# Kernel optimization log

Measured on AMD Instinct MI355X. Metric: run time of the kernel, lower is better.

Reference implementation:

```python
import jax, jax.numpy as jnp
import numpy as np
import math

B, I, H = 8192, 1024, 1024

def _uniform(key, shape, lo, hi):
    return jax.random.uniform(key, shape, dtype=jnp.float32, minval=lo, maxval=hi)

def setup_inputs() -> dict:
    key = jax.random.key(0)
    ks = jax.random.split(key, 14)
    bound = math.sqrt(1.0 / H)
    lo, hi = -bound, bound
    x = jax.random.normal(ks[0], (B, I), dtype=jnp.float32)
    hid = jax.random.normal(ks[1], (B, H), dtype=jnp.float32)
    # stacked params for gates [r, z, n]
    wx = jnp.stack([_uniform(ks[2 + i], (I, H), lo, hi) for i in range(3)])   # [3, I, H]
    wh = jnp.stack([_uniform(ks[5 + i], (H, H), lo, hi) for i in range(3)])   # [3, H, H]
    bx = jnp.stack([_uniform(ks[8 + i], (H,), lo, hi) for i in range(3)])     # [3, H]
    bh = jnp.stack([_uniform(ks[11 + i], (H,), lo, hi) for i in range(3)])    # [3, H]
    return {"x": x, "hid": hid, "wx": wx, "wh": wh, "bx": bx, "bh": bh}

def reference(x, hid, wx, wh, bx, bh):
    # Fused gate projections: one big matmul per source instead of 3 small ones.
    gx = jnp.einsum('bi,gih->bgh', x, wx) + bx[None]        # [B, 3, H]
    gh = jnp.einsum('bh,ghk->bgk', hid, wh) + bh[None]      # [B, 3, H]
    r = jax.nn.sigmoid(gx[:, 0] + gh[:, 0])
    z = jax.nn.sigmoid(gx[:, 1] + gh[:, 1])
    n = jnp.tanh(gx[:, 2] + r * gh[:, 2])
    next_hid = (1.0 - z) * n + z * hid
    return next_hid
```

## Files before the change

kernel.cpp:

```cpp
#include <hip/hip_runtime.h>
#include <hip/hip_bf16.h>

typedef __hip_bfloat16 bf16;
typedef unsigned short u16;
typedef __attribute__((ext_vector_type(8))) short bf16x8;
typedef __attribute__((ext_vector_type(4))) float f32x4;
typedef __attribute__((ext_vector_type(8))) unsigned short u16x8;

#define KD 1024
#define HD 1024
#define BSZ 8192
#define BM 128
#define BN 64
#define BK 32

__device__ __forceinline__ u16 f2b(float f) {
    return __builtin_bit_cast(u16, __float2bfloat16(f));
}

__device__ __forceinline__ void gload16(const void* g, void* smem, int lds_byte_off) {
    __builtin_amdgcn_global_load_lds(
        (const __attribute__((address_space(1))) void*)g,
        (__attribute__((address_space(3))) void*)((char*)smem + lds_byte_off),
        16, 0, 0);
}

__device__ __forceinline__ bf16x8 packfrag(float4 a, float4 b) {
    bf16x8 r;
    r[0] = (short)f2b(a.x); r[1] = (short)f2b(a.y);
    r[2] = (short)f2b(a.z); r[3] = (short)f2b(a.w);
    r[4] = (short)f2b(b.x); r[5] = (short)f2b(b.y);
    r[6] = (short)f2b(b.z); r[7] = (short)f2b(b.w);
    return r;
}

__global__ __launch_bounds__(256) void transpose_w(
    const float* __restrict__ wx, const float* __restrict__ wh, u16* __restrict__ wt)
{
    __shared__ u16 tile[64][65];
    const int g = blockIdx.z;
    const float* src = (g < 3) ? (wx + (size_t)g * KD * HD) : (wh + (size_t)(g - 3) * KD * HD);
    u16* dst = wt + (size_t)g * KD * HD;
    const int r0 = blockIdx.y * 64;
    const int c0 = blockIdx.x * 64;
    const int t = threadIdx.x;

    #pragma unroll
    for (int r = 0; r < 2; r++) {
        int idx = r * 256 + t;
        int row = idx >> 3, cc = idx & 7;
        const float* p = src + (size_t)(r0 + row) * HD + c0 + cc * 8;
        #pragma unroll
        for (int e = 0; e < 8; e++) tile[row][cc * 8 + e] = f2b(p[e]);
    }
    __syncthreads();
    #pragma unroll
    for (int r = 0; r < 2; r++) {
        int idx = r * 256 + t;
        int nrow = idx >> 3, kc = idx & 7;
        u16x8 v;
        #pragma unroll
        for (int e = 0; e < 8; e++) v[e] = tile[kc * 8 + e][nrow];
        *(u16x8*)(dst + (size_t)(c0 + nrow) * KD + r0 + kc * 8) = v;
    }
}

__global__ __launch_bounds__(256, 2) void gru_fused(
    const float* __restrict__ xf, const float* __restrict__ hf,
    const u16* __restrict__ wt,
    const float* __restrict__ bxf, const float* __restrict__ bhf,
    float* __restrict__ outf)
{
    __shared__ __align__(16) char smem[57344];
    float* fx = (float*)smem;
    float* fh = (float*)(smem + 16384);
    u16*   wl = (u16*)(smem + 32768);

    const int t    = threadIdx.x;
    const int lane = t & 63;
    const int w    = t >> 6;
    const int wm   = w >> 1, wn = w & 1;
    const int quad = lane >> 4;
    const int c16  = lane & 15;
    const int lin  = blockIdx.x;
    const int nblk = (lin & 7) * 2 + ((lin >> 3) & 1);
    const int mblk = lin >> 4;
    const int m0   = mblk * BM;
    const int n0   = nblk * BN;

    const int tq = t >> 3, tc = t & 7;
    const int csrc = tc ^ (tq & 7);
    const float* gx = xf + (size_t)(m0 + tq) * KD + csrc * 4;
    const float* gh = hf + (size_t)(m0 + tq) * KD + csrc * 4;
    const u16*   gw = wt + (size_t)(n0 + (t >> 2)) * KD + (t & 3) * 8;
    const int ldsl = w * 1024;

    f32x4 acc[4][4][2];
    #pragma unroll
    for (int a = 0; a < 4; a++)
        #pragma unroll
        for (int i = 0; i < 4; i++)
            #pragma unroll
            for (int j = 0; j < 2; j++)
                acc[a][i][j] = (f32x4){0.f, 0.f, 0.f, 0.f};

    int iA0[4], iA1[4];
    #pragma unroll
    for (int i = 0; i < 4; i++) {
        int ml = wm * 64 + i * 16 + c16;
        int s  = ml & 7;
        iA0[i] = ml * 32 + ((2 * quad)     ^ s) * 4;
        iA1[i] = ml * 32 + ((2 * quad + 1) ^ s) * 4;
    }
    int iW[2];
    #pragma unroll
    for (int j = 0; j < 2; j++) {
        int nl = wn * 32 + j * 16 + c16;
        iW[j] = nl * 32 + quad * 8;
    }

    for (int k0 = 0; k0 < KD; k0 += BK) {
        #pragma unroll
        for (int r = 0; r < 4; r++)
            gload16(gx + (size_t)(32 * r) * KD, smem, r * 4096 + ldsl);
        #pragma unroll
        for (int r = 0; r < 4; r++)
            gload16(gh + (size_t)(32 * r) * KD, smem, 16384 + r * 4096 + ldsl);
        #pragma unroll
        for (int g = 0; g < 6; g++)
            gload16(gw + (size_t)g * KD * HD, smem, 32768 + g * 4096 + ldsl);
        __syncthreads();
        gx += BK; gh += BK; gw += BK;

        bf16x8 ax[4], ah[4];
        #pragma unroll
        for (int i = 0; i < 4; i++) {
            float4 u0 = *(const float4*)&fx[iA0[i]];
            float4 u1 = *(const float4*)&fx[iA1[i]];
            float4 v0 = *(const float4*)&fh[iA0[i]];
            float4 v1 = *(const float4*)&fh[iA1[i]];
            ax[i] = packfrag(u0, u1);
            ah[i] = packfrag(v0, v1);
        }
        #pragma unroll
        for (int p = 0; p < 3; p++) {
            bf16x8 bwx[2], bwh[2];
            #pragma unroll
            for (int j = 0; j < 2; j++) {
                bwx[j] = *(const bf16x8*)&wl[p * 2048       + iW[j]];
                bwh[j] = *(const bf16x8*)&wl[(p + 3) * 2048 + iW[j]];
            }
            #pragma unroll
            for (int i = 0; i < 4; i++)
                #pragma unroll
                for (int j = 0; j < 2; j++) {
                    if (p < 2) {
                        acc[p][i][j] = __builtin_amdgcn_mfma_f32_16x16x32_bf16(ax[i], bwx[j], acc[p][i][j], 0, 0, 0);
                        acc[p][i][j] = __builtin_amdgcn_mfma_f32_16x16x32_bf16(ah[i], bwh[j], acc[p][i][j], 0, 0, 0);
                    } else {
                        acc[2][i][j] = __builtin_amdgcn_mfma_f32_16x16x32_bf16(ax[i], bwx[j], acc[2][i][j], 0, 0, 0);
                        acc[3][i][j] = __builtin_amdgcn_mfma_f32_16x16x32_bf16(ah[i], bwh[j], acc[3][i][j], 0, 0, 0);
                    }
                }
        }
        __syncthreads();
    }

    float bR[2], bZ[2], bXN[2], bHN[2];
    #pragma unroll
    for (int j = 0; j < 2; j++) {
        int col = n0 + wn * 32 + j * 16 + c16;
        bR[j]  = bxf[col]          + bhf[col];
        bZ[j]  = bxf[HD + col]     + bhf[HD + col];
        bXN[j] = bxf[2 * HD + col];
        bHN[j] = bhf[2 * HD + col];
    }
    #pragma unroll
    for (int i = 0; i < 4; i++)
        #pragma unroll
        for (int j = 0; j < 2; j++) {
            int col = n0 + wn * 32 + j * 16 + c16;
            #pragma unroll
            for (int r = 0; r < 4; r++) {
                int row = m0 + wm * 64 + i * 16 + quad * 4 + r;
                size_t idx = (size_t)row * HD + col;
                float vr = acc[0][i][j][r] + bR[j];
                vr = 1.f / (1.f + __expf(-vr));
                float vz = acc[1][i][j][r] + bZ[j];
                vz = 1.f / (1.f + __expf(-vz));
                float vn = (acc[2][i][j][r] + bXN[j]) + vr * (acc[3][i][j][r] + bHN[j]);
                float e2 = __expf(2.f * vn);
                vn = 1.f - 2.f / (e2 + 1.f);
                outf[idx] = (1.f - vz) * vn + vz * hf[idx];
            }
        }
}

extern "C" void kernel_launch(void* const* d_in, const int* in_sizes, int n_in,
                              void* d_out, int out_size, void* d_ws, size_t ws_size,
                              hipStream_t stream) {
    const float* x   = (const float*)d_in[0];
    const float* hid = (const float*)d_in[1];
    const float* wx  = (const float*)d_in[2];
    const float* wh  = (const float*)d_in[3];
    const float* bx  = (const float*)d_in[4];
    const float* bh  = (const float*)d_in[5];
    float* out = (float*)d_out;

    u16* wt = (u16*)d_ws;

    dim3 tgrid(HD / 64, KD / 64, 6);
    transpose_w<<<tgrid, 256, 0, stream>>>(wx, wh, wt);
    gru_fused<<<1024, 256, 0, stream>>>(x, hid, wt, bx, bh, out);
}
```

Measured before the change: 266.0 us.

## Pre-convert activations to bf16 and load A fragments directly from global

A merged prep kernel now converts x and hid to bf16 in workspace alongside the weight transpose. The GEMM kernel reads A fragments straight from global memory into registers instead of staging fp32 tiles in LDS, and LDS shrinks to the weight tiles only. The aim is to halve A-operand traffic in the main loop, remove per-iteration fp32-to-bf16 packing, and raise occupancy. The cost is an extra full pass writing and reading the bf16 activations, plus uncoalesced 16-byte per-lane global loads with no LDS reuse across the wn warps.

```diff
diff --git a/kernel.cpp b/kernel.cpp
--- a/kernel.cpp
+++ b/kernel.cpp
@@ -14,6 +14,9 @@
 #define BN 64
 #define BK 32
 
+#define WS_XB 12582912
+#define WS_HB 29360128
+
 __device__ __forceinline__ u16 f2b(float f) {
     return __builtin_bit_cast(u16, __float2bfloat16(f));
 }
@@ -25,57 +28,62 @@
         16, 0, 0);
 }
 
-__device__ __forceinline__ bf16x8 packfrag(float4 a, float4 b) {
-    bf16x8 r;
-    r[0] = (short)f2b(a.x); r[1] = (short)f2b(a.y);
-    r[2] = (short)f2b(a.z); r[3] = (short)f2b(a.w);
-    r[4] = (short)f2b(b.x); r[5] = (short)f2b(b.y);
-    r[6] = (short)f2b(b.z); r[7] = (short)f2b(b.w);
-    return r;
-}
-
-__global__ __launch_bounds__(256) void transpose_w(
-    const float* __restrict__ wx, const float* __restrict__ wh, u16* __restrict__ wt)
+__global__ __launch_bounds__(256) void prep_all(
+    const float* __restrict__ x, const float* __restrict__ h,
+    const float* __restrict__ wx, const float* __restrict__ wh,
+    u16* __restrict__ xb, u16* __restrict__ hb, u16* __restrict__ wt)
 {
     __shared__ u16 tile[64][65];
-    const int g = blockIdx.z;
-    const float* src = (g < 3) ? (wx + (size_t)g * KD * HD) : (wh + (size_t)(g - 3) * KD * HD);
-    u16* dst = wt + (size_t)g * KD * HD;
-    const int r0 = blockIdx.y * 64;
-    const int c0 = blockIdx.x * 64;
+    const int b = blockIdx.x;
     const int t = threadIdx.x;
-
-    #pragma unroll
-    for (int r = 0; r < 2; r++) {
-        int idx = r * 256 + t;
-        int row = idx >> 3, cc = idx & 7;
-        const float* p = src + (size_t)(r0 + row) * HD + c0 + cc * 8;
-        #pragma unroll
-        for (int e = 0; e < 8; e++) tile[row][cc * 8 + e] = f2b(p[e]);
+    if (b < 3072) {
+        const int g  = b >> 9;
+        const int r0 = ((b >> 4) & 15) * 64;
+        const int c0 = (b & 15) * 64;
+        const float* src = (g < 3) ? (wx + (size_t)g * KD * HD)
+                                   : (wh + (size_t)(g - 3) * KD * HD);
+        u16* dst = wt + (size_t)g * KD * HD;
+        #pragma unroll
+        for (int r = 0; r < 2; r++) {
+            int idx = r * 256 + t;
+            int row = idx >> 3, cc = idx & 7;
+            const float* p = src + (size_t)(r0 + row) * HD + c0 + cc * 8;
+            #pragma unroll
+            for (int e = 0; e < 8; e++) tile[row][cc * 8 + e] = f2b(p[e]);
+        }
+        __syncthreads();
+        #pragma unroll
+        for (int r = 0; r < 2; r++) {
+            int idx = r * 256 + t;
+            int nrow = idx >> 3, kc = idx & 7;
+            u16x8 v;
+            #pragma unroll
+            for (int e = 0; e < 8; e++) v[e] = tile[kc * 8 + e][nrow];
+            *(u16x8*)(dst + (size_t)(c0 + nrow) * KD + r0 + kc * 8) = v;
+        }
+    } else {
+        size_t off = ((size_t)(b - 3072) * 256 + t) * 8;
+        float4 a0 = *(const float4*)(x + off);
+        float4 a1 = *(const float4*)(x + off + 4);
+        float4 b0 = *(const float4*)(h + off);
+        float4 b1 = *(const float4*)(h + off + 4);
+        u16x8 vx, vh;
+        vx[0]=f2b(a0.x); vx[1]=f2b(a0.y); vx[2]=f2b(a0.z); vx[3]=f2b(a0.w);
+        vx[4]=f2b(a1.x); vx[5]=f2b(a1.y); vx[6]=f2b(a1.z); vx[7]=f2b(a1.w);
+        vh[0]=f2b(b0.x); vh[1]=f2b(b0.y); vh[2]=f2b(b0.z); vh[3]=f2b(b0.w);
+        vh[4]=f2b(b1.x); vh[5]=f2b(b1.y); vh[6]=f2b(b1.z); vh[7]=f2b(b1.w);
+        *(u16x8*)(xb + off) = vx;
+        *(u16x8*)(hb + off) = vh;
     }
-    __syncthreads();
-    #pragma unroll
-    for (int r = 0; r < 2; r++) {
-        int idx = r * 256 + t;
-        int nrow = idx >> 3, kc = idx & 7;
-        u16x8 v;
-        #pragma unroll
-        for (int e = 0; e < 8; e++) v[e] = tile[kc * 8 + e][nrow];
-        *(u16x8*)(dst + (size_t)(c0 + nrow) * KD + r0 + kc * 8) = v;
-    }
 }
 
 __global__ __launch_bounds__(256, 2) void gru_fused(
-    const float* __restrict__ xf, const float* __restrict__ hf,
+    const u16* __restrict__ xb, const u16* __restrict__ hb,
     const u16* __restrict__ wt,
     const float* __restrict__ bxf, const float* __restrict__ bhf,
-    float* __restrict__ outf)
+    const float* __restrict__ hidf, float* __restrict__ outf)
 {
-    __shared__ __align__(16) char smem[57344];
-    float* fx = (float*)smem;
-    float* fh = (float*)(smem + 16384);
-    u16*   wl = (u16*)(smem + 32768);
-
+    __shared__ u16 wl[12288];
     const int t    = threadIdx.x;
     const int lane = t & 63;
     const int w    = t >> 6;
@@ -88,12 +96,11 @@
     const int m0   = mblk * BM;
     const int n0   = nblk * BN;
 
-    const int tq = t >> 3, tc = t & 7;
-    const int csrc = tc ^ (tq & 7);
-    const float* gx = xf + (size_t)(m0 + tq) * KD + csrc * 4;
-    const float* gh = hf + (size_t)(m0 + tq) * KD + csrc * 4;
-    const u16*   gw = wt + (size_t)(n0 + (t >> 2)) * KD + (t & 3) * 8;
+    const u16* gw = wt + (size_t)(n0 + (t >> 2)) * KD + (t & 3) * 8;
     const int ldsl = w * 1024;
+
+    const u16* axp = xb + (size_t)(m0 + wm * 64 + c16) * KD + quad * 8;
+    const u16* ahp = hb + (size_t)(m0 + wm * 64 + c16) * KD + quad * 8;
 
     f32x4 acc[4][4][2];
     #pragma unroll
@@ -104,44 +111,24 @@
             for (int j = 0; j < 2; j++)
                 acc[a][i][j] = (f32x4){0.f, 0.f, 0.f, 0.f};
 
-    int iA0[4], iA1[4];
-    #pragma unroll
-    for (int i = 0; i < 4; i++) {
-        int ml = wm * 64 + i * 16 + c16;
-        int s  = ml & 7;
-        iA0[i] = ml * 32 + ((2 * quad)     ^ s) * 4;
-        iA1[i] = ml * 32 + ((2 * quad + 1) ^ s) * 4;
-    }
     int iW[2];
     #pragma unroll
-    for (int j = 0; j < 2; j++) {
-        int nl = wn * 32 + j * 16 + c16;
-        iW[j] = nl * 32 + quad * 8;
-    }
+    for (int j = 0; j < 2; j++)
+        iW[j] = (wn * 32 + j * 16 + c16) * 32 + quad * 8;
 
     for (int k0 = 0; k0 < KD; k0 += BK) {
         #pragma unroll
-        for (int r = 0; r < 4; r++)
-            gload16(gx + (size_t)(32 * r) * KD, smem, r * 4096 + ldsl);
-        #pragma unroll
-        for (int r = 0; r < 4; r++)
-            gload16(gh + (size_t)(32 * r) * KD, smem, 16384 + r * 4096 + ldsl);
-        #pragma unroll
         for (int g = 0; g < 6; g++)
-            gload16(gw + (size_t)g * KD * HD, smem, 32768 + g * 4096 + ldsl);
+            gload16(gw + (size_t)g * KD * HD, wl, g * 4096 + ldsl);
+        bf16x8 ax[4], ah[4];
+        #pragma unroll
+        for (int i = 0; i < 4; i++) {
+            ax[i] = *(const bf16x8*)(axp + (size_t)(i * 16) * KD);
+            ah[i] = *(const bf16x8*)(ahp + (size_t)(i * 16) * KD);
+        }
         __syncthreads();
-        gx += BK; gh += BK; gw += BK;
-
-        bf16x8 ax[4], ah[4];
-        #pragma unroll
-        for (int i = 0; i < 4; i++) {
-            float4 u0 = *(const float4*)&fx[iA0[i]];
-            float4 u1 = *(const float4*)&fx[iA1[i]];
-            float4 v0 = *(const float4*)&fh[iA0[i]];
-            float4 v1 = *(const float4*)&fh[iA1[i]];
-            ax[i] = packfrag(u0, u1);
-            ah[i] = packfrag(v0, v1);
-        }
+        gw += BK; axp += BK; ahp += BK;
+
         #pragma unroll
         for (int p = 0; p < 3; p++) {
             bf16x8 bwx[2], bwh[2];
@@ -191,7 +178,7 @@
                 float vn = (acc[2][i][j][r] + bXN[j]) + vr * (acc[3][i][j][r] + bHN[j]);
                 float e2 = __expf(2.f * vn);
                 vn = 1.f - 2.f / (e2 + 1.f);
-                outf[idx] = (1.f - vz) * vn + vz * hf[idx];
+                outf[idx] = (1.f - vz) * vn + vz * hidf[idx];
             }
         }
 }
@@ -207,9 +194,11 @@
     const float* bh  = (const float*)d_in[5];
     float* out = (float*)d_out;
 
-    u16* wt = (u16*)d_ws;
-
-    dim3 tgrid(HD / 64, KD / 64, 6);
-    transpose_w<<<tgrid, 256, 0, stream>>>(wx, wh, wt);
-    gru_fused<<<1024, 256, 0, stream>>>(x, hid, wt, bx, bh, out);
-}
+    char* ws = (char*)d_ws;
+    u16* wt = (u16*)ws;
+    u16* xb = (u16*)(ws + WS_XB);
+    u16* hb = (u16*)(ws + WS_HB);
+
+    prep_all<<<7168, 256, 0, stream>>>(x, hid, wx, wh, xb, hb, wt);
+    gru_fused<<<1024, 256, 0, stream>>>(xb, hb, wt, bx, bh, hid, out);
+}
```

New measurement: 300.8 us. 13.1% more time.
